# Performance work log

Measured on AMD Instinct MI355X. Metric: run time of the kernel, lower is better.

The kernel has to match this reference:

```python
import jax, jax.numpy as jnp
import numpy as np

HEADS = 16
DIM_HEAD = 64
EPS = 1e-12  # F.normalize default eps


def setup_inputs() -> dict:
    key = jax.random.key(0)
    k1, k2, k3 = jax.random.split(key, 3)
    b, n, dim = 2, 2048, 1024
    dim_inner = HEADS * DIM_HEAD
    x = jax.random.normal(k1, (b, n, dim), dtype=jnp.float32)
    gamma = jnp.ones((dim,), dtype=jnp.float32)
    w_qkv = jax.random.normal(k2, (dim, 3 * dim_inner), dtype=jnp.float32) * 0.02
    w_out = jax.random.normal(k3, (dim_inner, dim), dtype=jnp.float32) * 0.02
    return {"x": x, "gamma": gamma, "w_qkv": w_qkv, "w_out": w_out}


def reference(x, gamma, w_qkv, w_out):
    b, n, dim = x.shape
    h, d = HEADS, DIM_HEAD
    scale = d ** -0.5

    # RMSNorm (lucidrains): F.normalize(x, dim=-1) * dim**0.5 * gamma
    norm = jnp.sqrt(jnp.sum(x * x, axis=-1, keepdims=True))
    xn = x / jnp.maximum(norm, EPS) * (dim ** 0.5) * gamma

    # qkv projection -> [b, n, 3, h, d] -> q/k/v each [b, h, n, d]
    qkv = (xn @ w_qkv).reshape(b, n, 3, h, d)
    qkv = jnp.transpose(qkv, (2, 0, 3, 1, 4))
    q, k, v = qkv[0], qkv[1], qkv[2]

    q = q * scale
    sim = jnp.einsum('bhid,bhjd->bhij', q, k)  # [b, h, n, n]
    causal_mask = jnp.triu(jnp.ones((n, n), dtype=bool), k=1)
    mask_value = -jnp.finfo(sim.dtype).max
    sim = jnp.where(causal_mask, mask_value, sim)
    attn = jax.nn.softmax(sim, axis=-1)
    out = jnp.einsum('bhij,bhjd->bhid', attn, v)  # [b, h, n, d]

    out = jnp.transpose(out, (0, 2, 1, 3)).reshape(b, n, h * d)
    return out @ w_out
```

## Files before the change

kernel.cpp:

```cpp
#include <hip/hip_runtime.h>

typedef __attribute__((ext_vector_type(8))) short bf16x8;
typedef __attribute__((ext_vector_type(4))) short bf16x4;
typedef __attribute__((ext_vector_type(4))) float f32x4;

static __device__ __forceinline__ short f2bf(float f) {
    union { float f; unsigned u; } v; v.f = f;
    unsigned r = v.u + 0x7fffu + ((v.u >> 16) & 1u);
    return (short)(r >> 16);
}

static __device__ __forceinline__ float exp2_fast(float x) {
    float r; asm("v_exp_f32 %0, %1" : "=v"(r) : "v"(x)); return r;
}

static __device__ __forceinline__ void async_copy16(const short* g, short* l) {
    __builtin_amdgcn_global_load_lds((const __attribute__((address_space(1))) void*)g,
                                     (__attribute__((address_space(3))) void*)l,
                                     16, 0, 0);
}

#define BARX()                                            \
    do {                                                  \
        asm volatile("" ::: "memory");                    \
        __builtin_amdgcn_s_barrier();                     \
        __builtin_amdgcn_sched_barrier(0);                \
    } while (0)

#define HEADS 16
#define DHEAD 64
#define NSEQ  2048
#define DIM   1024
#define BATCH 2
#define ROWS  (BATCH * NSEQ)
#define NQKV  (3 * HEADS * DHEAD)

#define QSCALE 0.18033688f

__global__ __launch_bounds__(256) void prep_kernel(const float* __restrict__ x,
                                                   const float* __restrict__ gamma,
                                                   const float* __restrict__ w_qkv,
                                                   const float* __restrict__ w_out,
                                                   short* __restrict__ xn,
                                                   short* __restrict__ wqkvT,
                                                   short* __restrict__ woutT) {
    const int blk = blockIdx.x;
    const int t = threadIdx.x;
    __shared__ float tile[64][65];
    __shared__ float part[4];

    if (blk < 1024) {
        const float* in;  short* out;  int C, bx, by;
        if (blk < 768) { in = w_qkv; out = wqkvT; C = NQKV; bx = blk % 48; by = blk / 48; }
        else           { in = w_out; out = woutT; C = DIM;  bx = (blk - 768) & 15; by = (blk - 768) >> 4; }
        const int gx = bx * 64, gy = by * 64;
        const int lc4 = (t & 15) * 4;
        const int lr  = t >> 4;
#pragma unroll
        for (int p = 0; p < 4; ++p) {
            const float4 v = *(const float4*)&in[(size_t)(gy + p * 16 + lr) * C + gx + lc4];
            tile[p * 16 + lr][lc4 + 0] = v.x;
            tile[p * 16 + lr][lc4 + 1] = v.y;
            tile[p * 16 + lr][lc4 + 2] = v.z;
            tile[p * 16 + lr][lc4 + 3] = v.w;
        }
        __syncthreads();
        const int oc  = t >> 2;
        const int or4 = (t & 3) * 16;
#pragma unroll
        for (int j = 0; j < 4; ++j) {
            bf16x4 w;
#pragma unroll
            for (int r = 0; r < 4; ++r) w[r] = f2bf(tile[or4 + j * 4 + r][oc]);
            *(bf16x4*)&out[(size_t)(gx + oc) * DIM + gy + or4 + j * 4] = w;
        }
    } else {
        const int row = blk - 1024;
        const float4 v = ((const float4*)(x + (size_t)row * DIM))[t];
        float s = v.x * v.x + v.y * v.y + v.z * v.z + v.w * v.w;
#pragma unroll
        for (int off = 32; off > 0; off >>= 1) s += __shfl_down(s, off, 64);
        if ((t & 63) == 0) part[t >> 6] = s;
        __syncthreads();
        const float tot = part[0] + part[1] + part[2] + part[3];
        const float scale = 32.0f / fmaxf(sqrtf(tot), 1e-12f);
        const float4 g = ((const float4*)gamma)[t];
        bf16x4 o;
        o[0] = f2bf(v.x * scale * g.x);
        o[1] = f2bf(v.y * scale * g.y);
        o[2] = f2bf(v.z * scale * g.z);
        o[3] = f2bf(v.w * scale * g.w);
        *(bf16x4*)(xn + (size_t)row * DIM + t * 4) = o;
    }
}

__global__ __launch_bounds__(512, 2) void gemm_qkv(const short* __restrict__ A,
                                                   const short* __restrict__ Bt,
                                                   short* __restrict__ qkOut,
                                                   short* __restrict__ vtOut) {
    __shared__ alignas(16) short lA[2][256 * 64];
    __shared__ alignas(16) short lB[2][192 * 64];
    const int tid = threadIdx.x;
    const int lane = tid & 63, wid = tid >> 6;
    const int quad = lane >> 4, l16 = lane & 15;
    const int wm = wid >> 2, wn = wid & 3;

    int flat = blockIdx.x;
    flat = (flat & 7) * 32 + (flat >> 3);
    const int mb = (flat >> 4) * 256;
    const int nb = (flat & 15) * 192;

    f32x4 acc[8][3];
#pragma unroll
    for (int i = 0; i < 8; ++i)
#pragma unroll
        for (int j = 0; j < 3; ++j) acc[i][j] = (f32x4){0.f, 0.f, 0.f, 0.f};

    const int srow = tid >> 3;
    const int scol = (tid & 7) * 8;
    const int scolx = scol ^ ((srow & 7) * 8);

    auto stageA = [&](int kb, int buf) {
#pragma unroll
        for (int c = 0; c < 4; ++c) {
            const int row = c * 64 + srow;
            async_copy16(&A[(size_t)(mb + row) * 1024 + kb + scolx],
                         &lA[buf][row * 64 + scol]);
        }
    };
    auto stageB = [&](int kb, int buf) {
#pragma unroll
        for (int c = 0; c < 3; ++c) {
            const int row = c * 64 + srow;
            async_copy16(&Bt[(size_t)(nb + row) * 1024 + kb + scolx],
                         &lB[buf][row * 64 + scol]);
        }
    };
    auto rdA = [&](int buf, int mt, int kh) -> bf16x8 {
        const int row = wm * 128 + mt * 16 + l16;
        const int col = (kh * 32 + quad * 8) ^ ((row & 7) * 8);
        return *(const bf16x8*)&lA[buf][row * 64 + col];
    };
    auto rdB = [&](int buf, int nt, int kh) -> bf16x8 {
        const int row = wn * 48 + nt * 16 + l16;
        const int col = (kh * 32 + quad * 8) ^ ((row & 7) * 8);
        return *(const bf16x8*)&lB[buf][row * 64 + col];
    };

    stageA(0, 0);
    stageB(0, 0);
    asm volatile("s_waitcnt vmcnt(0)" ::: "memory");
    BARX();

    int cur = 0;
    for (int kt = 0; kt < 16; ++kt) {
        bf16x8 a[4][2], b01[2][2], b2[2];
#pragma unroll
        for (int mt = 0; mt < 4; ++mt)
#pragma unroll
            for (int kh = 0; kh < 2; ++kh) a[mt][kh] = rdA(cur, mt, kh);
#pragma unroll
        for (int nt = 0; nt < 2; ++nt)
#pragma unroll
            for (int kh = 0; kh < 2; ++kh) b01[nt][kh] = rdB(cur, nt, kh);
        if (kt < 15) {
            stageA((kt + 1) * 64, cur ^ 1);
            stageB((kt + 1) * 64, cur ^ 1);
        }
        BARX();
        __builtin_amdgcn_s_setprio(1);
#pragma unroll
        for (int kh = 0; kh < 2; ++kh)
#pragma unroll
            for (int mt = 0; mt < 4; ++mt)
#pragma unroll
                for (int nt = 0; nt < 2; ++nt)
                    acc[mt][nt] = __builtin_amdgcn_mfma_f32_16x16x32_bf16(
                        a[mt][kh], b01[nt][kh], acc[mt][nt], 0, 0, 0);
        __builtin_amdgcn_s_setprio(0);
#pragma unroll
        for (int kh = 0; kh < 2; ++kh) b2[kh] = rdB(cur, 2, kh);
        BARX();
        __builtin_amdgcn_s_setprio(1);
#pragma unroll
        for (int kh = 0; kh < 2; ++kh)
#pragma unroll
            for (int mt = 0; mt < 4; ++mt)
                acc[mt][2] = __builtin_amdgcn_mfma_f32_16x16x32_bf16(
                    a[mt][kh], b2[kh], acc[mt][2], 0, 0, 0);
        __builtin_amdgcn_s_setprio(0);
#pragma unroll
        for (int mt = 0; mt < 4; ++mt)
#pragma unroll
            for (int kh = 0; kh < 2; ++kh) a[mt][kh] = rdA(cur, mt + 4, kh);
        BARX();
        __builtin_amdgcn_s_setprio(1);
#pragma unroll
        for (int kh = 0; kh < 2; ++kh)
#pragma unroll
            for (int mt = 0; mt < 4; ++mt)
                acc[mt + 4][2] = __builtin_amdgcn_mfma_f32_16x16x32_bf16(
                    a[mt][kh], b2[kh], acc[mt + 4][2], 0, 0, 0);
        __builtin_amdgcn_s_setprio(0);
        asm volatile("s_waitcnt vmcnt(0)" ::: "memory");
        BARX();
        __builtin_amdgcn_s_setprio(1);
#pragma unroll
        for (int kh = 0; kh < 2; ++kh)
#pragma unroll
            for (int mt = 0; mt < 4; ++mt)
#pragma unroll
                for (int nt = 0; nt < 2; ++nt)
                    acc[mt + 4][nt] = __builtin_amdgcn_mfma_f32_16x16x32_bf16(
                        a[mt][kh], b01[nt][kh], acc[mt + 4][nt], 0, 0, 0);
        __builtin_amdgcn_s_setprio(0);
        cur ^= 1;
    }

#pragma unroll
    for (int mt = 0; mt < 8; ++mt) {
#pragma unroll
        for (int nt = 0; nt < 3; ++nt) {
            const int grow0 = mb + wm * 128 + mt * 16 + quad * 4;
            const int gcol  = nb + wn * 48 + nt * 16 + l16;
            const int s3 = gcol >> 10, rem = gcol & 1023;
            const int hh = rem >> 6, dd = rem & 63;
            const int bb = grow0 >> 11, npos0 = grow0 & 2047;
            if (s3 == 2) {
                bf16x4 vw;
#pragma unroll
                for (int r = 0; r < 4; ++r) vw[r] = f2bf(acc[mt][nt][r]);
                *(bf16x4*)&vtOut[((size_t)(bb * 16 + hh) * 64 + dd) * 2048 + npos0] = vw;
            } else {
                const float sc = (s3 == 0) ? QSCALE : 1.0f;
#pragma unroll
                for (int r = 0; r < 4; ++r)
                    qkOut[(size_t)((s3 * 32 + bb * 16 + hh) * 2048 + npos0 + r) * 64 + dd] =
                        f2bf(acc[mt][nt][r] * sc);
            }
        }
    }
}

__global__ __launch_bounds__(256, 3) void gemm_out(const short* __restrict__ A,
                                                   const short* __restrict__ Bt,
                                                   float* __restrict__ Cout) {
    __shared__ alignas(16) short lA2[2][128 * 64];
    __shared__ alignas(16) short lB2[2][64 * 64];
    const int tid = threadIdx.x;
    const int lane = tid & 63, wid = tid >> 6;
    const int quad = lane >> 4, l16 = lane & 15;

    const int nx = 16;
    int flat = blockIdx.y * nx + blockIdx.x;
    flat = (flat & 7) * 64 + (flat >> 3);
    const int mb = (flat / nx) * 128, nb = (flat % nx) * 64;

    f32x4 acc[2][4];
#pragma unroll
    for (int i = 0; i < 2; ++i)
#pragma unroll
        for (int j = 0; j < 4; ++j) acc[i][j] = (f32x4){0.f, 0.f, 0.f, 0.f};

    auto stage = [&](int kb, int buf) {
#pragma unroll
        for (int p = 0; p < 4; ++p) {
            const int ck = p * 256 + tid;
            const int ar = ck >> 3, as_ = ck & 7;
            async_copy16(&A[(size_t)(mb + ar) * 1024 + kb + ((as_ ^ (ar & 7)) * 8)],
                         &lA2[buf][ck * 8]);
        }
#pragma unroll
        for (int p = 0; p < 2; ++p) {
            const int cb = p * 256 + tid;
            const int br = cb >> 3, bs = cb & 7;
            async_copy16(&Bt[(size_t)(nb + br) * 1024 + kb + ((bs ^ (br & 7)) * 8)],
                         &lB2[buf][cb * 8]);
        }
    };

    stage(0, 0);
    __syncthreads();

    int cur = 0;
    for (int kt = 0; kt < 16; ++kt) {
        if (kt + 1 < 16) stage((kt + 1) * 64, cur ^ 1);

        bf16x8 af[2][2], bfr[4][2];
#pragma unroll
        for (int mt = 0; mt < 2; ++mt) {
            const int row = wid * 32 + mt * 16 + l16;
#pragma unroll
            for (int kh = 0; kh < 2; ++kh)
                af[mt][kh] = *(const bf16x8*)&lA2[cur][row * 64 +
                                                      (((kh * 4 + quad) ^ (row & 7)) * 8)];
        }
#pragma unroll
        for (int nt = 0; nt < 4; ++nt) {
            const int row = nt * 16 + l16;
#pragma unroll
            for (int kh = 0; kh < 2; ++kh)
                bfr[nt][kh] = *(const bf16x8*)&lB2[cur][row * 64 +
                                                       (((kh * 4 + quad) ^ (row & 7)) * 8)];
        }
#pragma unroll
        for (int kh = 0; kh < 2; ++kh)
#pragma unroll
            for (int mt = 0; mt < 2; ++mt)
#pragma unroll
                for (int nt = 0; nt < 4; ++nt)
                    acc[mt][nt] = __builtin_amdgcn_mfma_f32_16x16x32_bf16(
                        af[mt][kh], bfr[nt][kh], acc[mt][nt], 0, 0, 0);
        __syncthreads();
        cur ^= 1;
    }

#pragma unroll
    for (int mt = 0; mt < 2; ++mt) {
#pragma unroll
        for (int nt = 0; nt < 4; ++nt) {
            const int grow0 = mb + wid * 32 + mt * 16 + quad * 4;
            const int gcol  = nb + nt * 16 + l16;
#pragma unroll
            for (int r = 0; r < 4; ++r)
                Cout[(size_t)(grow0 + r) * DIM + gcol] = acc[mt][nt][r];
        }
    }
}

__global__ __launch_bounds__(256, 2) void attn_kernel(const short* __restrict__ qg,
                                                      const short* __restrict__ kg,
                                                      const short* __restrict__ vtg,
                                                      short* __restrict__ og) {
    const int tid = threadIdx.x;
    const int wid = tid >> 6, lane = tid & 63;
    const int quad = lane >> 4, l16 = lane & 15;
    const int blk = blockIdx.x;
    const int qt = (blk < 256) ? (15 - (blk >> 5)) : ((blk - 256) >> 5);
    const int bh = blk & 31;
    const size_t base = (size_t)bh * (NSEQ * DHEAD);
    const int bb = bh >> 4, hh = bh & 15;
    const int qbase = qt * 128 + wid * 32;
    const int steps = qt + 1;

    __shared__ alignas(16) short kT[2][128 * 64];
    __shared__ alignas(16) short vT[2][64 * 128];

    auto stage = [&](int s, int buf) {
        const int kb = s * 128;
#pragma unroll
        for (int p = 0; p < 4; ++p) {
            const int ck = p * 256 + tid;
            const int kr = ck >> 3, ksl = ck & 7;
            async_copy16(&kg[base + (size_t)(kb + kr) * 64 + ((ksl ^ (kr & 7)) * 8)],
                         &kT[buf][ck * 8]);
        }
#pragma unroll
        for (int p = 0; p < 4; ++p) {
            const int cv = p * 256 + tid;
            const int vr = cv >> 4, vsl = cv & 15;
            async_copy16(&vtg[base + (size_t)vr * 2048 + kb + ((vsl ^ (vr & 15)) * 8)],
                         &vT[buf][cv * 8]);
        }
    };

    bf16x8 qf[2][2];
#pragma unroll
    for (int qn = 0; qn < 2; ++qn)
#pragma unroll
        for (int kh = 0; kh < 2; ++kh)
            qf[qn][kh] = *(const bf16x8*)&qg[base + (size_t)(qbase + qn * 16 + l16) * DHEAD +
                                            kh * 32 + quad * 8];

    float li[2] = {0.f, 0.f};
    f32x4 accO[2][4];
#pragma unroll
    for (int qn = 0; qn < 2; ++qn)
#pragma unroll
        for (int nc = 0; nc < 4; ++nc) accO[qn][nc] = (f32x4){0.f, 0.f, 0.f, 0.f};

    auto tile_step = [&](int buf, int s) {
        const int kb = s * 128;
        f32x4 sf[2][2][4];
#pragma unroll
        for (int h = 0; h < 2; ++h) {
#pragma unroll
            for (int m = 0; m < 4; ++m) {
                const int row = h * 64 + m * 16 + l16;
                const int rb = row * 64;
                const int sw = (row & 7) * 8;
                const bf16x8 kf0 = *(const bf16x8*)&kT[buf][rb + ((quad * 8) ^ sw)];
                const bf16x8 kf1 = *(const bf16x8*)&kT[buf][rb + ((32 + quad * 8) ^ sw)];
#pragma unroll
                for (int qn = 0; qn < 2; ++qn) {
                    f32x4 z = (f32x4){0.f, 0.f, 0.f, 0.f};
                    z = __builtin_amdgcn_mfma_f32_16x16x32_bf16(kf0, qf[qn][0], z, 0, 0, 0);
                    sf[h][qn][m] = __builtin_amdgcn_mfma_f32_16x16x32_bf16(kf1, qf[qn][1], z,
                                                                           0, 0, 0);
                }
            }
        }
#pragma unroll
        for (int h = 0; h < 2; ++h) {
            if (kb + h * 64 + 64 > qbase) {
#pragma unroll
                for (int qn = 0; qn < 2; ++qn) {
                    const int myq = qbase + qn * 16 + l16;
#pragma unroll
                    for (int m = 0; m < 4; ++m)
#pragma unroll
                        for (int r = 0; r < 4; ++r)
                            if (kb + h * 64 + m * 16 + quad * 4 + r > myq)
                                sf[h][qn][m][r] = -3.0e38f;
                }
            }
        }
        bf16x8 pf[2][4];
#pragma unroll
        for (int h = 0; h < 2; ++h) {
            unsigned c0[2][4], c1[2][4];
#pragma unroll
            for (int qn = 0; qn < 2; ++qn) {
                float rs = 0.f;
#pragma unroll
                for (int m = 0; m < 4; ++m) {
                    const float p0 = exp2_fast(sf[h][qn][m][0]);
                    const float p1 = exp2_fast(sf[h][qn][m][1]);
                    const float p2 = exp2_fast(sf[h][qn][m][2]);
                    const float p3 = exp2_fast(sf[h][qn][m][3]);
                    rs += (p0 + p1) + (p2 + p3);
                    asm("v_cvt_pk_bf16_f32 %0, %1, %2" : "=v"(c0[qn][m]) : "v"(p0), "v"(p1));
                    asm("v_cvt_pk_bf16_f32 %0, %1, %2" : "=v"(c1[qn][m]) : "v"(p2), "v"(p3));
                }
                li[qn] += rs;
            }
#pragma unroll
            for (int qn = 0; qn < 2; ++qn)
#pragma unroll
                for (int ks = 0; ks < 2; ++ks) {
                    unsigned a0 = c0[qn][2 * ks], b0 = c0[qn][2 * ks + 1];
                    unsigned a1 = c1[qn][2 * ks], b1 = c1[qn][2 * ks + 1];
                    asm("v_permlane32_swap_b32 %0, %1" : "+v"(a0), "+v"(b0));
                    asm("v_permlane16_swap_b32 %0, %1" : "+v"(a0), "+v"(b0));
                    asm("v_permlane32_swap_b32 %0, %1" : "+v"(a1), "+v"(b1));
                    asm("v_permlane16_swap_b32 %0, %1" : "+v"(a1), "+v"(b1));
                    union { bf16x8 v; unsigned u[4]; } t8;
                    t8.u[0] = a0; t8.u[1] = a1; t8.u[2] = b0; t8.u[3] = b1;
                    pf[qn][h * 2 + ks] = t8.v;
                }
        }
#pragma unroll
        for (int nc = 0; nc < 4; ++nc) {
            const int row = nc * 16 + l16;
            const int rb = row * 128;
#pragma unroll
            for (int ks = 0; ks < 4; ++ks) {
                const bf16x8 vf =
                    *(const bf16x8*)&vT[buf][rb + (((ks * 4 + quad) ^ (row & 15)) * 8)];
#pragma unroll
                for (int qn = 0; qn < 2; ++qn)
                    accO[qn][nc] = __builtin_amdgcn_mfma_f32_16x16x32_bf16(vf, pf[qn][ks],
                                                                          accO[qn][nc],
                                                                          0, 0, 0);
            }
        }
    };

    stage(0, 0);
    __syncthreads();
    int cur = 0;
    for (int s = 0; s < steps; ++s) {
        if (s + 1 < steps) stage(s + 1, cur ^ 1);
        tile_step(cur, s);
        __syncthreads();
        cur ^= 1;
    }

#pragma unroll
    for (int qn = 0; qn < 2; ++qn) {
        li[qn] += __shfl_xor(li[qn], 16, 64);
        li[qn] += __shfl_xor(li[qn], 32, 64);
        const float inv = 1.0f / li[qn];
        const int npos = qbase + qn * 16 + l16;
#pragma unroll
        for (int nc = 0; nc < 4; ++nc) {
            bf16x4 ow;
#pragma unroll
            for (int r = 0; r < 4; ++r) ow[r] = f2bf(accO[qn][nc][r] * inv);
            *(bf16x4*)&og[(size_t)(bb * 2048 + npos) * 1024 + hh * 64 + nc * 16 + quad * 4] = ow;
        }
    }
}

extern "C" void kernel_launch(void* const* d_in, const int* in_sizes, int n_in,
                              void* d_out, int out_size, void* d_ws, size_t ws_size,
                              hipStream_t stream) {
    const float* x     = (const float*)d_in[0];
    const float* gamma = (const float*)d_in[1];
    const float* w_qkv = (const float*)d_in[2];
    const float* w_out = (const float*)d_in[3];
    float* out = (float*)d_out;
    char* ws = (char*)d_ws;

    short* xn     = (short*)(ws);
    short* wqkvT  = (short*)(ws + 8388608);
    short* woutT  = (short*)(ws + 14680064);
    short* q      = (short*)(ws + 16777216);
    short* k      = q + 32 * 2048 * 64;
    short* vt     = k + 32 * 2048 * 64;
    short* attn   = (short*)(ws + 41943040);

    prep_kernel<<<5120, 256, 0, stream>>>(x, gamma, w_qkv, w_out, xn, wqkvT, woutT);
    gemm_qkv<<<256, 512, 0, stream>>>(xn, wqkvT, q, vt);
    attn_kernel<<<512, 256, 0, stream>>>(q, k, vt, attn);
    gemm_out<<<dim3(16, 32), 256, 0, stream>>>(attn, woutT, out);
}
```

Before: 163.4 us.

## Shrink QKV GEMM block tile to 128x192 with 4 warps and 512 blocks

Retiles the QKV projection GEMM from 256x192 tiles with 8 warps to 128x192 tiles with 4 warps, launching twice as many blocks. Each warp now computes a 64x96 sub-tile, using 4x6 accumulators instead of 8x3. The inner loop is restructured into two MFMA phases per k-step instead of four. The aim is better CU occupancy and balance (512 blocks over the device's CUs, more resident blocks per CU from smaller LDS use), at the cost of less A/B reuse per block and more global traffic for B.

```diff
diff --git a/kernel.cpp b/kernel.cpp
--- a/kernel.cpp
+++ b/kernel.cpp
@@ -94,27 +94,27 @@
     }
 }
 
-__global__ __launch_bounds__(512, 2) void gemm_qkv(const short* __restrict__ A,
+__global__ __launch_bounds__(256, 2) void gemm_qkv(const short* __restrict__ A,
                                                    const short* __restrict__ Bt,
                                                    short* __restrict__ qkOut,
                                                    short* __restrict__ vtOut) {
-    __shared__ alignas(16) short lA[2][256 * 64];
+    __shared__ alignas(16) short lA[2][128 * 64];
     __shared__ alignas(16) short lB[2][192 * 64];
     const int tid = threadIdx.x;
     const int lane = tid & 63, wid = tid >> 6;
     const int quad = lane >> 4, l16 = lane & 15;
-    const int wm = wid >> 2, wn = wid & 3;
+    const int wm = wid >> 1, wn = wid & 1;
 
     int flat = blockIdx.x;
-    flat = (flat & 7) * 32 + (flat >> 3);
-    const int mb = (flat >> 4) * 256;
+    flat = (flat & 7) * 64 + (flat >> 3);
+    const int mb = (flat >> 4) * 128;
     const int nb = (flat & 15) * 192;
 
-    f32x4 acc[8][3];
-#pragma unroll
-    for (int i = 0; i < 8; ++i)
-#pragma unroll
-        for (int j = 0; j < 3; ++j) acc[i][j] = (f32x4){0.f, 0.f, 0.f, 0.f};
+    f32x4 acc[4][6];
+#pragma unroll
+    for (int i = 0; i < 4; ++i)
+#pragma unroll
+        for (int j = 0; j < 6; ++j) acc[i][j] = (f32x4){0.f, 0.f, 0.f, 0.f};
 
     const int srow = tid >> 3;
     const int scol = (tid & 7) * 8;
@@ -123,26 +123,26 @@
     auto stageA = [&](int kb, int buf) {
 #pragma unroll
         for (int c = 0; c < 4; ++c) {
-            const int row = c * 64 + srow;
+            const int row = c * 32 + srow;
             async_copy16(&A[(size_t)(mb + row) * 1024 + kb + scolx],
                          &lA[buf][row * 64 + scol]);
         }
     };
     auto stageB = [&](int kb, int buf) {
 #pragma unroll
-        for (int c = 0; c < 3; ++c) {
-            const int row = c * 64 + srow;
+        for (int c = 0; c < 6; ++c) {
+            const int row = c * 32 + srow;
             async_copy16(&Bt[(size_t)(nb + row) * 1024 + kb + scolx],
                          &lB[buf][row * 64 + scol]);
         }
     };
     auto rdA = [&](int buf, int mt, int kh) -> bf16x8 {
-        const int row = wm * 128 + mt * 16 + l16;
+        const int row = wm * 64 + mt * 16 + l16;
         const int col = (kh * 32 + quad * 8) ^ ((row & 7) * 8);
         return *(const bf16x8*)&lA[buf][row * 64 + col];
     };
     auto rdB = [&](int buf, int nt, int kh) -> bf16x8 {
-        const int row = wn * 48 + nt * 16 + l16;
+        const int row = wn * 96 + nt * 16 + l16;
         const int col = (kh * 32 + quad * 8) ^ ((row & 7) * 8);
         return *(const bf16x8*)&lB[buf][row * 64 + col];
     };
@@ -154,15 +154,15 @@
 
     int cur = 0;
     for (int kt = 0; kt < 16; ++kt) {
-        bf16x8 a[4][2], b01[2][2], b2[2];
+        bf16x8 a[4][2], b[3][2];
 #pragma unroll
         for (int mt = 0; mt < 4; ++mt)
 #pragma unroll
             for (int kh = 0; kh < 2; ++kh) a[mt][kh] = rdA(cur, mt, kh);
 #pragma unroll
-        for (int nt = 0; nt < 2; ++nt)
-#pragma unroll
-            for (int kh = 0; kh < 2; ++kh) b01[nt][kh] = rdB(cur, nt, kh);
+        for (int nt = 0; nt < 3; ++nt)
+#pragma unroll
+            for (int kh = 0; kh < 2; ++kh) b[nt][kh] = rdB(cur, nt, kh);
         if (kt < 15) {
             stageA((kt + 1) * 64, cur ^ 1);
             stageB((kt + 1) * 64, cur ^ 1);
@@ -174,55 +174,36 @@
 #pragma unroll
             for (int mt = 0; mt < 4; ++mt)
 #pragma unroll
-                for (int nt = 0; nt < 2; ++nt)
+                for (int nt = 0; nt < 3; ++nt)
                     acc[mt][nt] = __builtin_amdgcn_mfma_f32_16x16x32_bf16(
-                        a[mt][kh], b01[nt][kh], acc[mt][nt], 0, 0, 0);
+                        a[mt][kh], b[nt][kh], acc[mt][nt], 0, 0, 0);
         __builtin_amdgcn_s_setprio(0);
 #pragma unroll
-        for (int kh = 0; kh < 2; ++kh) b2[kh] = rdB(cur, 2, kh);
+        for (int nt = 0; nt < 3; ++nt)
+#pragma unroll
+            for (int kh = 0; kh < 2; ++kh) b[nt][kh] = rdB(cur, nt + 3, kh);
         BARX();
         __builtin_amdgcn_s_setprio(1);
 #pragma unroll
         for (int kh = 0; kh < 2; ++kh)
 #pragma unroll
             for (int mt = 0; mt < 4; ++mt)
-                acc[mt][2] = __builtin_amdgcn_mfma_f32_16x16x32_bf16(
-                    a[mt][kh], b2[kh], acc[mt][2], 0, 0, 0);
-        __builtin_amdgcn_s_setprio(0);
-#pragma unroll
-        for (int mt = 0; mt < 4; ++mt)
-#pragma unroll
-            for (int kh = 0; kh < 2; ++kh) a[mt][kh] = rdA(cur, mt + 4, kh);
-        BARX();
-        __builtin_amdgcn_s_setprio(1);
-#pragma unroll
-        for (int kh = 0; kh < 2; ++kh)
-#pragma unroll
-            for (int mt = 0; mt < 4; ++mt)
-                acc[mt + 4][2] = __builtin_amdgcn_mfma_f32_16x16x32_bf16(
-                    a[mt][kh], b2[kh], acc[mt + 4][2], 0, 0, 0);
+#pragma unroll
+                for (int nt = 0; nt < 3; ++nt)
+                    acc[mt][nt + 3] = __builtin_amdgcn_mfma_f32_16x16x32_bf16(
+                        a[mt][kh], b[nt][kh], acc[mt][nt + 3], 0, 0, 0);
         __builtin_amdgcn_s_setprio(0);
         asm volatile("s_waitcnt vmcnt(0)" ::: "memory");
         BARX();
-        __builtin_amdgcn_s_setprio(1);
-#pragma unroll
-        for (int kh = 0; kh < 2; ++kh)
-#pragma unroll
-            for (int mt = 0; mt < 4; ++mt)
-#pragma unroll
-                for (int nt = 0; nt < 2; ++nt)
-                    acc[mt + 4][nt] = __builtin_amdgcn_mfma_f32_16x16x32_bf16(
-                        a[mt][kh], b01[nt][kh], acc[mt + 4][nt], 0, 0, 0);
-        __builtin_amdgcn_s_setprio(0);
         cur ^= 1;
     }
 
 #pragma unroll
-    for (int mt = 0; mt < 8; ++mt) {
-#pragma unroll
-        for (int nt = 0; nt < 3; ++nt) {
-            const int grow0 = mb + wm * 128 + mt * 16 + quad * 4;
-            const int gcol  = nb + wn * 48 + nt * 16 + l16;
+    for (int mt = 0; mt < 4; ++mt) {
+#pragma unroll
+        for (int nt = 0; nt < 6; ++nt) {
+            const int grow0 = mb + wm * 64 + mt * 16 + quad * 4;
+            const int gcol  = nb + wn * 96 + nt * 16 + l16;
             const int s3 = gcol >> 10, rem = gcol & 1023;
             const int hh = rem >> 6, dd = rem & 63;
             const int bb = grow0 >> 11, npos0 = grow0 & 2047;
@@ -511,7 +492,7 @@
     short* attn   = (short*)(ws + 41943040);
 
     prep_kernel<<<5120, 256, 0, stream>>>(x, gamma, w_qkv, w_out, xn, wqkvT, woutT);
-    gemm_qkv<<<256, 512, 0, stream>>>(xn, wqkvT, q, vt);
+    gemm_qkv<<<512, 256, 0, stream>>>(xn, wqkvT, q, vt);
     attn_kernel<<<512, 256, 0, stream>>>(q, k, vt, attn);
     gemm_out<<<dim3(16, 32), 256, 0, stream>>>(attn, woutT, out);
 }
```

After: 161.1 us, median of 2. Within noise of the previous version (-1.4%).
